# Kernel tuning notes

Measured on AMD Instinct MI355X. Metric: run time of the kernel, lower is better.

Reference implementation:

```python
import jax, jax.numpy as jnp
import numpy as np

# Paired binary-tree layout over 20 inputs: widths 20->10->5->3->2->1.
# Odd trailing element is carried through unchanged. Node counts per layer
# sum to 19 nodes per tree; 19 trees total.
LAYER_WIDTHS = [20, 10, 5, 3, 2]  # widths at the input of each pairing layer
NODE_COUNTS = [10, 5, 2, 1, 1]    # pairs formed at each layer (sum = 19)
EPS = 1e-6


def setup_inputs() -> dict:
    key = jax.random.key(0)
    k1, k2, k3, k4 = jax.random.split(key, 4)
    B = 1_000_000
    p1 = jax.random.randint(k1, (B,), 0, 10)
    p2 = jax.random.randint(k2, (B,), 0, 10)
    c20 = jax.random.uniform(k3, (B, 20), dtype=jnp.float32)  # fuzzy truth values in [0,1]
    # raw andness params: one per node (19) per tree (19)
    w_raw = jax.random.normal(k4, (19, 19), dtype=jnp.float32)
    return {"p1": p1, "p2": p2, "c20": c20, "w_raw": w_raw}


def _multi_tree_forward(c20, w_raw):
    B = c20.shape[0]
    T = 19  # number of trees
    # andness in (0,1): convex mix between AND (min) and OR (max)
    w = jax.nn.sigmoid(w_raw)  # [T, 19]
    # all 19 trees see the same 20D input -> vectorize trees as a dim
    x = jnp.broadcast_to(c20[:, None, :], (B, T, 20))  # [B, T, 20]
    off = 0
    for width, n in zip(LAYER_WIDTHS, NODE_COUNTS):
        a = x[:, :, 0:2 * n:2]   # left children  [B, T, n]
        b = x[:, :, 1:2 * n:2]   # right children [B, T, n]
        wn = w[:, off:off + n][None, :, :]  # [1, T, n]
        y = wn * jnp.minimum(a, b) + (1.0 - wn) * jnp.maximum(a, b)
        if width % 2 == 1:  # carry the unpaired trailing element through
            y = jnp.concatenate([y, x[:, :, -1:]], axis=-1)
        x = y
        off += n
    out = x[:, :, 0]  # [B, 19] root of each tree
    return jnp.clip(out, EPS, 1.0 - EPS)


def reference(p1, p2, c20, w_raw):
    # p1/p2 are part of the original signature but unused by the forward math
    return _multi_tree_forward(c20, w_raw)
```

## Files before the change

### kernel.cpp

```cpp
#include <hip/hip_runtime.h>

#define EPS_F 1e-6f
#define BLK   256

__global__ void sigmoid_w_kernel(const float* __restrict__ w_raw,
                                 float* __restrict__ w) {
    int i = threadIdx.x;
    if (i < 361) {
        w[i] = 1.0f / (1.0f + expf(-w_raw[i]));
    }
}

__device__ __forceinline__ float mixf(float a, float b, float wv) {
    float mn = fminf(a, b);
    float mx = fmaxf(a, b);
    return fmaf(wv, mn - mx, mx);
}

__device__ __forceinline__ float clampf(float r) {
    return fminf(fmaxf(r, EPS_F), 1.0f - EPS_F);
}

__global__ __launch_bounds__(BLK) void tree_forward_kernel(
    const float* __restrict__ c20,
    const float* __restrict__ w,
    float* __restrict__ out,
    int B)
{
    __shared__ float so[BLK * 19];

    const int tid = threadIdx.x;
    const long long S0 = (long long)blockIdx.x * BLK;
    const long long s  = S0 + tid;

    float x[20];
    if (s < B) {
        const float4* p = reinterpret_cast<const float4*>(c20 + s * 20);
        #pragma unroll
        for (int q = 0; q < 5; ++q) {
            float4 v = p[q];
            x[4*q+0] = v.x; x[4*q+1] = v.y; x[4*q+2] = v.z; x[4*q+3] = v.w;
        }
    } else {
        #pragma unroll
        for (int i = 0; i < 20; ++i) x[i] = 0.0f;
    }

    float mx[10], d[10];
    #pragma unroll
    for (int k = 0; k < 10; ++k) {
        float a = x[2*k], b = x[2*k+1];
        float mn = fminf(a, b);
        mx[k] = fmaxf(a, b);
        d[k]  = mn - mx[k];
    }

    float* __restrict__ o = &so[tid * 19];

    #pragma unroll
    for (int tp = 0; tp < 9; ++tp) {
        const int t0 = 2 * tp, t1 = 2 * tp + 1;
        const float* wr0 = w + t0 * 19;
        const float* wr1 = w + t1 * 19;

        float y0[10], y1[10];
        #pragma unroll
        for (int k = 0; k < 10; ++k) {
            y0[k] = fmaf(wr0[k], d[k], mx[k]);
            y1[k] = fmaf(wr1[k], d[k], mx[k]);
        }

        float z0[5], z1[5];
        #pragma unroll
        for (int k = 0; k < 5; ++k) {
            z0[k] = mixf(y0[2*k], y0[2*k+1], wr0[10 + k]);
            z1[k] = mixf(y1[2*k], y1[2*k+1], wr1[10 + k]);
        }

        float u00 = mixf(z0[0], z0[1], wr0[15]);
        float u01 = mixf(z0[2], z0[3], wr0[16]);
        float u10 = mixf(z1[0], z1[1], wr1[15]);
        float u11 = mixf(z1[2], z1[3], wr1[16]);

        float v0 = mixf(u00, u01, wr0[17]);
        float v1 = mixf(u10, u11, wr1[17]);

        float r0 = mixf(v0, z0[4], wr0[18]);
        float r1 = mixf(v1, z1[4], wr1[18]);

        o[t0] = clampf(r0);
        o[t1] = clampf(r1);
    }

    {
        const float* wr = w + 18 * 19;
        float y[10];
        #pragma unroll
        for (int k = 0; k < 10; ++k)
            y[k] = fmaf(wr[k], d[k], mx[k]);
        float z[5];
        #pragma unroll
        for (int k = 0; k < 5; ++k)
            z[k] = mixf(y[2*k], y[2*k+1], wr[10 + k]);
        float u0 = mixf(z[0], z[1], wr[15]);
        float u1 = mixf(z[2], z[3], wr[16]);
        float v0 = mixf(u0, u1, wr[17]);
        float r  = mixf(v0, z[4], wr[18]);
        o[18] = clampf(r);
    }

    __syncthreads();

    const long long nDw    = (long long)B * 19;
    const long long baseDw = S0 * 19;
    const float4* ls = reinterpret_cast<const float4*>(so);

    #pragma unroll
    for (int i = tid; i < (BLK * 19) / 4; i += BLK) {
        long long g = baseDw + (long long)i * 4;
        if (g + 3 < nDw) {
            *reinterpret_cast<float4*>(out + g) = ls[i];
        } else if (g < nDw) {
            float4 v = ls[i];
            out[g] = v.x;
            if (g + 1 < nDw) out[g + 1] = v.y;
            if (g + 2 < nDw) out[g + 2] = v.z;
        }
    }
}

extern "C" void kernel_launch(void* const* d_in, const int* in_sizes, int n_in,
                              void* d_out, int out_size, void* d_ws, size_t ws_size,
                              hipStream_t stream) {
    const float* c20   = (const float*)d_in[2];
    const float* w_raw = (const float*)d_in[3];
    float* out = (float*)d_out;
    float* w   = (float*)d_ws;

    int B = in_sizes[0];

    sigmoid_w_kernel<<<1, 384, 0, stream>>>(w_raw, w);

    int grid = (B + BLK - 1) / BLK;
    tree_forward_kernel<<<grid, BLK, 0, stream>>>(c20, w, out, B);
}
```

Measured before the change: 155.4 us.

## Process two samples per thread with packed float2 math and nontemporal stores

Each thread now handles two samples, packing them into 2-wide float vectors so the tree mix arithmetic can map to packed FP32 instructions (v_pk_fma/v_pk_mul) and each weight load is amortized over two samples. The grid is halved, and output is staged through shared memory in two rounds with extra barriers, using nontemporal vector stores. The clamp is replaced with a single med3 instruction and 64-bit index math with 32-bit. In exchange, register pressure rises (an extra 19-float buffer), fewer waves are launched, and B*19 now must fit in an int.

```diff
diff --git a/kernel.cpp b/kernel.cpp
--- a/kernel.cpp
+++ b/kernel.cpp
@@ -2,6 +2,9 @@
 
 #define EPS_F 1e-6f
 #define BLK   256
+
+typedef float v2f __attribute__((ext_vector_type(2)));
+typedef float v4f __attribute__((ext_vector_type(4)));
 
 __global__ void sigmoid_w_kernel(const float* __restrict__ w_raw,
                                  float* __restrict__ w) {
@@ -11,14 +14,19 @@
     }
 }
 
-__device__ __forceinline__ float mixf(float a, float b, float wv) {
-    float mn = fminf(a, b);
-    float mx = fmaxf(a, b);
-    return fmaf(wv, mn - mx, mx);
+__device__ __forceinline__ v2f vsplat(float s) {
+    v2f r; r.x = s; r.y = s; return r;
+}
+
+__device__ __forceinline__ v2f vmix(v2f a, v2f b, float wv) {
+    v2f mn, mx;
+    mn.x = fminf(a.x, b.x); mn.y = fminf(a.y, b.y);
+    mx.x = fmaxf(a.x, b.x); mx.y = fmaxf(a.y, b.y);
+    return vsplat(wv) * (mn - mx) + mx;
 }
 
 __device__ __forceinline__ float clampf(float r) {
-    return fminf(fmaxf(r, EPS_F), 1.0f - EPS_F);
+    return __builtin_amdgcn_fmed3f(r, EPS_F, 1.0f - EPS_F);
 }
 
 __global__ __launch_bounds__(BLK) void tree_forward_kernel(
@@ -30,101 +38,102 @@
     __shared__ float so[BLK * 19];
 
     const int tid = threadIdx.x;
-    const long long S0 = (long long)blockIdx.x * BLK;
-    const long long s  = S0 + tid;
+    const int S0  = blockIdx.x * (2 * BLK);
+    const int sA  = S0 + tid;
+    const int sB  = S0 + BLK + tid;
 
-    float x[20];
-    if (s < B) {
-        const float4* p = reinterpret_cast<const float4*>(c20 + s * 20);
+    v2f d[10], mx[10];
+    {
+        const float4* pA = reinterpret_cast<const float4*>(c20 + (size_t)sA * 20);
+        const float4* pB = reinterpret_cast<const float4*>(c20 + (size_t)sB * 20);
+        const bool vA = (sA < B), vB = (sB < B);
         #pragma unroll
         for (int q = 0; q < 5; ++q) {
-            float4 v = p[q];
-            x[4*q+0] = v.x; x[4*q+1] = v.y; x[4*q+2] = v.z; x[4*q+3] = v.w;
+            float4 a4 = vA ? pA[q] : make_float4(0.f, 0.f, 0.f, 0.f);
+            float4 b4 = vB ? pB[q] : make_float4(0.f, 0.f, 0.f, 0.f);
+            {
+                v2f a, b;
+                a.x = a4.x; a.y = b4.x;
+                b.x = a4.y; b.y = b4.y;
+                v2f mn;
+                mn.x       = fminf(a.x, b.x); mn.y       = fminf(a.y, b.y);
+                mx[2*q].x  = fmaxf(a.x, b.x); mx[2*q].y  = fmaxf(a.y, b.y);
+                d[2*q] = mn - mx[2*q];
+            }
+            {
+                v2f a, b;
+                a.x = a4.z; a.y = b4.z;
+                b.x = a4.w; b.y = b4.w;
+                v2f mn;
+                mn.x        = fminf(a.x, b.x); mn.y        = fminf(a.y, b.y);
+                mx[2*q+1].x = fmaxf(a.x, b.x); mx[2*q+1].y = fmaxf(a.y, b.y);
+                d[2*q+1] = mn - mx[2*q+1];
+            }
         }
-    } else {
-        #pragma unroll
-        for (int i = 0; i < 20; ++i) x[i] = 0.0f;
     }
 
-    float mx[10], d[10];
-    #pragma unroll
-    for (int k = 0; k < 10; ++k) {
-        float a = x[2*k], b = x[2*k+1];
-        float mn = fminf(a, b);
-        mx[k] = fmaxf(a, b);
-        d[k]  = mn - mx[k];
-    }
-
+    float oB[19];
     float* __restrict__ o = &so[tid * 19];
 
     #pragma unroll
-    for (int tp = 0; tp < 9; ++tp) {
-        const int t0 = 2 * tp, t1 = 2 * tp + 1;
-        const float* wr0 = w + t0 * 19;
-        const float* wr1 = w + t1 * 19;
-
-        float y0[10], y1[10];
-        #pragma unroll
-        for (int k = 0; k < 10; ++k) {
-            y0[k] = fmaf(wr0[k], d[k], mx[k]);
-            y1[k] = fmaf(wr1[k], d[k], mx[k]);
-        }
-
-        float z0[5], z1[5];
+    for (int t = 0; t < 19; ++t) {
+        const float* wr = w + t * 19;
+        v2f z[5];
         #pragma unroll
         for (int k = 0; k < 5; ++k) {
-            z0[k] = mixf(y0[2*k], y0[2*k+1], wr0[10 + k]);
-            z1[k] = mixf(y1[2*k], y1[2*k+1], wr1[10 + k]);
+            v2f ya = vsplat(wr[2*k    ]) * d[2*k    ] + mx[2*k    ];
+            v2f yb = vsplat(wr[2*k + 1]) * d[2*k + 1] + mx[2*k + 1];
+            z[k] = vmix(ya, yb, wr[10 + k]);
         }
-
-        float u00 = mixf(z0[0], z0[1], wr0[15]);
-        float u01 = mixf(z0[2], z0[3], wr0[16]);
-        float u10 = mixf(z1[0], z1[1], wr1[15]);
-        float u11 = mixf(z1[2], z1[3], wr1[16]);
-
-        float v0 = mixf(u00, u01, wr0[17]);
-        float v1 = mixf(u10, u11, wr1[17]);
-
-        float r0 = mixf(v0, z0[4], wr0[18]);
-        float r1 = mixf(v1, z1[4], wr1[18]);
-
-        o[t0] = clampf(r0);
-        o[t1] = clampf(r1);
-    }
-
-    {
-        const float* wr = w + 18 * 19;
-        float y[10];
-        #pragma unroll
-        for (int k = 0; k < 10; ++k)
-            y[k] = fmaf(wr[k], d[k], mx[k]);
-        float z[5];
-        #pragma unroll
-        for (int k = 0; k < 5; ++k)
-            z[k] = mixf(y[2*k], y[2*k+1], wr[10 + k]);
-        float u0 = mixf(z[0], z[1], wr[15]);
-        float u1 = mixf(z[2], z[3], wr[16]);
-        float v0 = mixf(u0, u1, wr[17]);
-        float r  = mixf(v0, z[4], wr[18]);
-        o[18] = clampf(r);
+        v2f u0 = vmix(z[0], z[1], wr[15]);
+        v2f u1 = vmix(z[2], z[3], wr[16]);
+        v2f v  = vmix(u0, u1, wr[17]);
+        v2f r  = vmix(v, z[4], wr[18]);
+        o[t]  = clampf(r.x);
+        oB[t] = clampf(r.y);
     }
 
     __syncthreads();
 
-    const long long nDw    = (long long)B * 19;
-    const long long baseDw = S0 * 19;
-    const float4* ls = reinterpret_cast<const float4*>(so);
+    const int nDw = B * 19;
+    const v4f* ls = reinterpret_cast<const v4f*>(so);
+
+    {
+        const int baseDw = S0 * 19;
+        #pragma unroll
+        for (int i = tid; i < (BLK * 19) / 4; i += BLK) {
+            int g = baseDw + i * 4;
+            if (g + 3 < nDw) {
+                __builtin_nontemporal_store(ls[i], reinterpret_cast<v4f*>(out + g));
+            } else if (g < nDw) {
+                v4f v4 = ls[i];
+                out[g] = v4.x;
+                if (g + 1 < nDw) out[g + 1] = v4.y;
+                if (g + 2 < nDw) out[g + 2] = v4.z;
+            }
+        }
+    }
+
+    __syncthreads();
 
     #pragma unroll
-    for (int i = tid; i < (BLK * 19) / 4; i += BLK) {
-        long long g = baseDw + (long long)i * 4;
-        if (g + 3 < nDw) {
-            *reinterpret_cast<float4*>(out + g) = ls[i];
-        } else if (g < nDw) {
-            float4 v = ls[i];
-            out[g] = v.x;
-            if (g + 1 < nDw) out[g + 1] = v.y;
-            if (g + 2 < nDw) out[g + 2] = v.z;
+    for (int t = 0; t < 19; ++t) o[t] = oB[t];
+
+    __syncthreads();
+
+    {
+        const int baseDw = (S0 + BLK) * 19;
+        #pragma unroll
+        for (int i = tid; i < (BLK * 19) / 4; i += BLK) {
+            int g = baseDw + i * 4;
+            if (g + 3 < nDw) {
+                __builtin_nontemporal_store(ls[i], reinterpret_cast<v4f*>(out + g));
+            } else if (g < nDw) {
+                v4f v4 = ls[i];
+                out[g] = v4.x;
+                if (g + 1 < nDw) out[g + 1] = v4.y;
+                if (g + 2 < nDw) out[g + 2] = v4.z;
+            }
         }
     }
 }
@@ -141,6 +150,6 @@
 
     sigmoid_w_kernel<<<1, 384, 0, stream>>>(w_raw, w);
 
-    int grid = (B + BLK - 1) / BLK;
+    int grid = (B + 2 * BLK - 1) / (2 * BLK);
     tree_forward_kernel<<<grid, BLK, 0, stream>>>(c20, w, out, B);
 }
```

Result: slower. 159.8 us (+2.9%).

## Stage input tile through LDS with coalesced loads and nontemporal output stores

Applied to the files above, without the earlier changes.

Input rows are now loaded cooperatively as contiguous 16-byte vectors into a shared-memory tile, replacing per-thread strided 80-byte reads, and each thread then reads its own row from LDS. Output stores become nontemporal, the clamp uses a single med3 instruction, indexing switches to 32-bit ints, and launch bounds request 4 blocks per CU. The cost is an extra 20 KB of LDS per block plus one more barrier, which may limit occupancy. Possible LDS bank conflicts on the 80-byte-stride row reads are another risk.

```diff
diff --git a/kernel.cpp b/kernel.cpp
--- a/kernel.cpp
+++ b/kernel.cpp
@@ -2,6 +2,8 @@
 
 #define EPS_F 1e-6f
 #define BLK   256
+
+typedef float v4f __attribute__((ext_vector_type(4)));
 
 __global__ void sigmoid_w_kernel(const float* __restrict__ w_raw,
                                  float* __restrict__ w) {
@@ -18,41 +20,57 @@
 }
 
 __device__ __forceinline__ float clampf(float r) {
-    return fminf(fmaxf(r, EPS_F), 1.0f - EPS_F);
+    return __builtin_amdgcn_fmed3f(r, EPS_F, 1.0f - EPS_F);
 }
 
-__global__ __launch_bounds__(BLK) void tree_forward_kernel(
+__global__ __launch_bounds__(BLK, 4) void tree_forward_kernel(
     const float* __restrict__ c20,
     const float* __restrict__ w,
     float* __restrict__ out,
     int B)
 {
+    __shared__ float si[BLK * 20];
     __shared__ float so[BLK * 19];
 
     const int tid = threadIdx.x;
-    const long long S0 = (long long)blockIdx.x * BLK;
-    const long long s  = S0 + tid;
+    const int S0  = blockIdx.x * BLK;
 
-    float x[20];
-    if (s < B) {
-        const float4* p = reinterpret_cast<const float4*>(c20 + s * 20);
+    {
+        const v4f* g4 = reinterpret_cast<const v4f*>(c20) + (size_t)S0 * 5;
+        v4f* s4 = reinterpret_cast<v4f*>(si);
+        const int lim4  = B * 5;
+        const int base4 = S0 * 5;
+        #pragma unroll
+        for (int j = 0; j < 5; ++j) {
+            int idx = tid + j * BLK;
+            v4f v;
+            if (base4 + idx < lim4) {
+                v = g4[idx];
+            } else {
+                v.x = 0.f; v.y = 0.f; v.z = 0.f; v.w = 0.f;
+            }
+            s4[idx] = v;
+        }
+    }
+    __syncthreads();
+
+    float mx[10], d[10];
+    {
+        const v4f* r4 = reinterpret_cast<const v4f*>(si + tid * 20);
         #pragma unroll
         for (int q = 0; q < 5; ++q) {
-            float4 v = p[q];
-            x[4*q+0] = v.x; x[4*q+1] = v.y; x[4*q+2] = v.z; x[4*q+3] = v.w;
+            v4f v = r4[q];
+            {
+                float mn = fminf(v.x, v.y);
+                mx[2*q] = fmaxf(v.x, v.y);
+                d[2*q]  = mn - mx[2*q];
+            }
+            {
+                float mn = fminf(v.z, v.w);
+                mx[2*q+1] = fmaxf(v.z, v.w);
+                d[2*q+1]  = mn - mx[2*q+1];
+            }
         }
-    } else {
-        #pragma unroll
-        for (int i = 0; i < 20; ++i) x[i] = 0.0f;
-    }
-
-    float mx[10], d[10];
-    #pragma unroll
-    for (int k = 0; k < 10; ++k) {
-        float a = x[2*k], b = x[2*k+1];
-        float mn = fminf(a, b);
-        mx[k] = fmaxf(a, b);
-        d[k]  = mn - mx[k];
     }
 
     float* __restrict__ o = &so[tid * 19];
@@ -111,20 +129,20 @@
 
     __syncthreads();
 
-    const long long nDw    = (long long)B * 19;
-    const long long baseDw = S0 * 19;
-    const float4* ls = reinterpret_cast<const float4*>(so);
+    const int nDw    = B * 19;
+    const int baseDw = S0 * 19;
+    const v4f* ls = reinterpret_cast<const v4f*>(so);
 
     #pragma unroll
     for (int i = tid; i < (BLK * 19) / 4; i += BLK) {
-        long long g = baseDw + (long long)i * 4;
+        int g = baseDw + i * 4;
         if (g + 3 < nDw) {
-            *reinterpret_cast<float4*>(out + g) = ls[i];
+            __builtin_nontemporal_store(ls[i], reinterpret_cast<v4f*>(out + g));
         } else if (g < nDw) {
-            float4 v = ls[i];
-            out[g] = v.x;
-            if (g + 1 < nDw) out[g + 1] = v.y;
-            if (g + 2 < nDw) out[g + 2] = v.z;
+            v4f v4 = ls[i];
+            out[g] = v4.x;
+            if (g + 1 < nDw) out[g + 1] = v4.y;
+            if (g + 2 < nDw) out[g + 2] = v4.z;
         }
     }
 }
```

Result: slower. 159.7 us (+2.8%).
